# Kernel optimization log

Hardware: AMD Instinct MI355X
Metric: run time of the kernel (lower is better)

Reference implementation:

```python
import jax, jax.numpy as jnp
import numpy as np

EPS = float(np.finfo(np.float32).eps)  # torch.finfo(float32).eps


def _inv2x2(M):
    """Elementwise inverse of 2x2 complex matrices. M: (..., 2, 2) complex."""
    det = M[..., 0, 0] * M[..., 1, 1] - M[..., 0, 1] * M[..., 1, 0]
    # matches torch _inv: conj(z) / |z|^2
    inv_det = jnp.conj(det) / (jnp.abs(det) ** 2)
    row0 = jnp.stack([inv_det * M[..., 1, 1], -inv_det * M[..., 0, 1]], axis=-1)
    row1 = jnp.stack([-inv_det * M[..., 1, 0], inv_det * M[..., 0, 0]], axis=-1)
    return jnp.stack([row0, row1], axis=-2)


def _em(y, x, iterations):
    # y: (F, B, C, 2, S) real/imag; x: (F, B, C, 2)
    yc = y[..., 0, :] + 1j * y[..., 1, :]          # (F, B, C, S) complex
    xc = x[..., 0] + 1j * x[..., 1]                # (F, B, C)   complex
    nb_channels = yc.shape[2]
    reg = jnp.sqrt(jnp.asarray(EPS, jnp.float32)) * jnp.eye(
        nb_channels, dtype=yc.dtype)               # sqrt(eps)*I regularizer
    v = jnp.mean(jnp.abs(yc) ** 2, axis=2)         # (F, B, S)
    R = jnp.einsum('fbcs,fbds->bcds', yc, jnp.conj(yc))
    for _ in range(iterations):
        # E-step: PSD = channel-average power spectrogram
        v = jnp.mean(jnp.abs(yc) ** 2, axis=2)     # (F, B, S)
        # spatial covariance: sum_f y y^H / (eps + sum_f v)  -> (B, C, C, S)
        R = jnp.einsum('fbcs,fbds->bcds', yc, jnp.conj(yc))
        R = R / (EPS + jnp.sum(v, axis=0))[:, None, None, :]
        # mixture covariance Cxx = sqrt(eps)*I + sum_j v_j R_j  -> (F, B, C, C)
        Cxx = reg[None, None] + jnp.einsum('fbs,bcds->fbcd', v, R)
        inv_Cxx = _inv2x2(Cxx)
        # Wiener gain G_j = v_j * R_j @ inv_Cxx  -> (F, B, C, C, S)
        gain = jnp.einsum('fbs,bcks,fbkd->fbcds', v, R, inv_Cxx)
        # apply filter: y_j = G_j @ x
        yc = jnp.einsum('fbcds,fbd->fbcs', gain, xc)
    y_out = jnp.stack([jnp.real(yc), jnp.imag(yc)], axis=-2)   # (F, B, C, 2, S)
    R_out = jnp.stack([jnp.real(R), jnp.imag(R)], axis=-2)     # (B, C, C, 2, S)
    return y_out, v, R_out


def setup_inputs() -> dict:
    key = jax.random.key(0)
    k1, k2 = jax.random.split(key)
    F, B, C, S = 1000, 2049, 2, 4
    y = jax.random.normal(k1, (F, B, C, 2, S), dtype=jnp.float32)
    x = jax.random.normal(k2, (F, B, C, 2), dtype=jnp.float32)
    return {"y": y, "x": x, "iterations": 2}


def reference(y, x, iterations):
    return _em(y, x, iterations)
```

## Files before the change

### kernel.cpp

```cpp
#include <hip/hip_runtime.h>

#define FDIM 1000
#define BDIM 2049
#define NTH  256
#define FS   8
#define FT   125
#define BT   16
#define NBT  129
#define GRID (NBT * FS)

#define V_OFF 32784000ull
#define R_OFF 40980000ull

#define P2_OFF ((size_t)BDIM * FS * 20)

#define EPSF 1.1920928955078125e-07f
#define REGC 3.4526698300124393e-04f

__global__ __launch_bounds__(NTH) void k1_power(
    const float* __restrict__ y, float* __restrict__ v, float* __restrict__ part1)
{
    const int btile = blockIdx.x / FS;
    const int fs    = blockIdx.x % FS;
    const int tid   = threadIdx.x;
    const int bs    = tid & 15;
    const int fi    = tid >> 4;
    const int wid   = tid >> 6;
    const int b     = btile * BT + bs;
    const bool vb   = (b < BDIM);

    float acc[20];
    #pragma unroll
    for (int j = 0; j < 20; ++j) acc[j] = 0.f;

    const int f0 = fs * FT;
    #pragma unroll
    for (int ii = 0; ii < 8; ++ii) {
        const int fo = ii * 16 + fi;
        if (fo < FT && vb) {
            const int f = f0 + fo;
            const size_t e = (size_t)f * BDIM + b;
            const float4* yp = reinterpret_cast<const float4*>(y) + e * 4;
            float4 a0 = yp[0], a1 = yp[1], a2 = yp[2], a3 = yp[3];
            float y0r[4] = {a0.x,a0.y,a0.z,a0.w};
            float y0i[4] = {a1.x,a1.y,a1.z,a1.w};
            float y1r[4] = {a2.x,a2.y,a2.z,a2.w};
            float y1i[4] = {a3.x,a3.y,a3.z,a3.w};
            float vv[4];
            #pragma unroll
            for (int s = 0; s < 4; ++s) {
                const float p0 = y0r[s]*y0r[s] + y0i[s]*y0i[s];
                const float p1 = y1r[s]*y1r[s] + y1i[s]*y1i[s];
                vv[s] = 0.5f * (p0 + p1);
                acc[s]    += p0;
                acc[4+s]  += p1;
                acc[8+s]  += y0r[s]*y1r[s] + y0i[s]*y1i[s];
                acc[12+s] += y0i[s]*y1r[s] - y0r[s]*y1i[s];
                acc[16+s] += vv[s];
            }
            reinterpret_cast<float4*>(v)[e] = make_float4(vv[0], vv[1], vv[2], vv[3]);
        }
    }
    #pragma unroll
    for (int j = 0; j < 20; ++j) {
        float t = acc[j];
        t += __shfl_xor(t, 16);
        t += __shfl_xor(t, 32);
        acc[j] = t;
    }
    __shared__ float red[4][16][20];
    if ((tid & 63) < 16) {
        #pragma unroll
        for (int j = 0; j < 20; ++j) red[wid][bs][j] = acc[j];
    }
    __syncthreads();
    for (int idx = tid; idx < 320; idx += NTH) {
        const int bss = idx & 15, j = idx >> 4;
        const int bb = btile * BT + bss;
        if (bb < BDIM)
            part1[((size_t)bb * FS + fs) * 20 + j] =
                red[0][bss][j] + red[1][bss][j] + red[2][bss][j] + red[3][bss][j];
    }
}

__global__ __launch_bounds__(NTH) void k3_em(
    const float* __restrict__ x, float* __restrict__ v,
    const float* __restrict__ part1, float* __restrict__ part2,
    const int* __restrict__ itp)
{
    const int btile = blockIdx.x / FS;
    const int fs    = blockIdx.x % FS;
    const int tid   = threadIdx.x;
    const int bs    = tid & 15;
    const int fi    = tid >> 4;
    const int wid   = tid >> 6;
    const int b     = btile * BT + bs;
    const bool vb   = (b < BDIM);
    const int iters = itp[0];

    __shared__ float rsumS[16][20];
    __shared__ float rnormS[16][16];
    for (int idx = tid; idx < 320; idx += NTH) {
        const int bss = idx & 15, j = idx >> 4;
        const int bb = btile * BT + bss;
        float s = 0.f;
        if (bb < BDIM) {
            #pragma unroll
            for (int q = 0; q < FS; ++q) s += part1[((size_t)bb * FS + q) * 20 + j];
        }
        rsumS[bss][j] = s;
    }
    __syncthreads();
    {
        const int bss = tid & 15, j = tid >> 4;
        rnormS[bss][j] = rsumS[bss][j] / (EPSF + rsumS[bss][16 + (j & 3)]);
    }
    __syncthreads();

    if (iters <= 1) {
        for (int idx = tid; idx < 320; idx += NTH) {
            const int bss = idx & 15, j = idx >> 4;
            const int bb = btile * BT + bss;
            if (bb < BDIM)
                part2[((size_t)bb * FS + fs) * 20 + j] = (fs == 0) ? rsumS[bss][j] : 0.f;
        }
        return;
    }

    float rn00[4], rn11[4], rn01r[4], rn01i[4];
    #pragma unroll
    for (int s = 0; s < 4; ++s) {
        rn00[s]=rnormS[bs][s]; rn11[s]=rnormS[bs][4+s];
        rn01r[s]=rnormS[bs][8+s]; rn01i[s]=rnormS[bs][12+s];
    }

    float acc[20];
    #pragma unroll
    for (int j = 0; j < 20; ++j) acc[j] = 0.f;

    const int f0 = fs * FT;
    #pragma unroll
    for (int ii = 0; ii < 8; ++ii) {
        const int fo = ii * 16 + fi;
        if (fo < FT && vb) {
            const int f = f0 + fo;
            const size_t e = (size_t)f * BDIM + b;
            float4 vv4 = reinterpret_cast<const float4*>(v)[e];
            float4 xv  = reinterpret_cast<const float4*>(x)[e];
            float v1[4] = {vv4.x, vv4.y, vv4.z, vv4.w};
            float c00 = REGC, c11 = REGC, c01r = 0.f, c01i = 0.f;
            #pragma unroll
            for (int s = 0; s < 4; ++s) {
                c00  += v1[s]*rn00[s];
                c11  += v1[s]*rn11[s];
                c01r += v1[s]*rn01r[s];
                c01i += v1[s]*rn01i[s];
            }
            const float det  = c00*c11 - (c01r*c01r + c01i*c01i);
            const float invd = det / (det*det);
            const float i00 = invd*c11, i11 = invd*c00;
            const float i01r = -invd*c01r, i01i = -invd*c01i;
            const float xr0 = xv.x, xi0 = xv.y, xr1 = xv.z, xi1 = xv.w;
            const float w0r = i00*xr0 + (i01r*xr1 - i01i*xi1);
            const float w0i = i00*xi0 + (i01r*xi1 + i01i*xr1);
            const float w1r = (i01r*xr0 + i01i*xi0) + i11*xr1;
            const float w1i = (i01r*xi0 - i01i*xr0) + i11*xi1;
            float v2[4];
            #pragma unroll
            for (int s = 0; s < 4; ++s) {
                const float vs = v1[s];
                const float y0r = vs*(rn00[s]*w0r + (rn01r[s]*w1r - rn01i[s]*w1i));
                const float y0i = vs*(rn00[s]*w0i + (rn01r[s]*w1i + rn01i[s]*w1r));
                const float y1r = vs*((rn01r[s]*w0r + rn01i[s]*w0i) + rn11[s]*w1r);
                const float y1i = vs*((rn01r[s]*w0i - rn01i[s]*w0r) + rn11[s]*w1i);
                const float p0 = y0r*y0r + y0i*y0i;
                const float p1 = y1r*y1r + y1i*y1i;
                v2[s] = 0.5f*(p0 + p1);
                acc[s]    += p0;
                acc[4+s]  += p1;
                acc[8+s]  += y0r*y1r + y0i*y1i;
                acc[12+s] += y0i*y1r - y0r*y1i;
                acc[16+s] += v2[s];
            }
            reinterpret_cast<float4*>(v)[e] = make_float4(v2[0], v2[1], v2[2], v2[3]);
        }
    }
    #pragma unroll
    for (int j = 0; j < 20; ++j) {
        float t = acc[j];
        t += __shfl_xor(t, 16);
        t += __shfl_xor(t, 32);
        acc[j] = t;
    }
    __shared__ float red[4][16][20];
    if ((tid & 63) < 16) {
        #pragma unroll
        for (int j = 0; j < 20; ++j) red[wid][bs][j] = acc[j];
    }
    __syncthreads();
    for (int idx = tid; idx < 320; idx += NTH) {
        const int bss = idx & 15, j = idx >> 4;
        const int bb = btile * BT + bss;
        if (bb < BDIM)
            part2[((size_t)bb * FS + fs) * 20 + j] =
                red[0][bss][j] + red[1][bss][j] + red[2][bss][j] + red[3][bss][j];
    }
}

__global__ __launch_bounds__(NTH) void k5_final(
    const float* __restrict__ y, const float* __restrict__ x, const float* __restrict__ v,
    const float* __restrict__ part2, float* __restrict__ yout, float* __restrict__ Rout,
    const int* __restrict__ itp)
{
    const int btile = blockIdx.x / FS;
    const int fs    = blockIdx.x % FS;
    const int tid   = threadIdx.x;
    const int bs    = tid & 15;
    const int fi    = tid >> 4;
    const int b     = btile * BT + bs;
    const bool vb   = (b < BDIM);
    const int iters = itp[0];

    __shared__ float rsumS[16][20];
    __shared__ float rnormS[16][16];
    for (int idx = tid; idx < 320; idx += NTH) {
        const int bss = idx & 15, j = idx >> 4;
        const int bb = btile * BT + bss;
        float s = 0.f;
        if (bb < BDIM) {
            #pragma unroll
            for (int q = 0; q < FS; ++q) s += part2[((size_t)bb * FS + q) * 20 + j];
        }
        rsumS[bss][j] = s;
    }
    __syncthreads();
    {
        const int bss = tid & 15, j = tid >> 4;
        rnormS[bss][j] = rsumS[bss][j] / (EPSF + rsumS[bss][16 + (j & 3)]);
    }
    __syncthreads();

    if (fs == 0) {
        for (int idx = tid; idx < 512; idx += NTH) {
            const int bss = idx >> 5, r = idx & 31;
            const int bb = btile * BT + bss;
            if (bb < BDIM) {
                const int c = (r>>4)&1, d = (r>>3)&1, ri = (r>>2)&1, s = r&3;
                const bool raw = (iters == 0);
                float val;
                if (c == d) {
                    val = ri ? 0.f : (raw ? rsumS[bss][(c?4:0)+s] : rnormS[bss][(c?4:0)+s]);
                } else {
                    const float re = raw ? rsumS[bss][8+s]  : rnormS[bss][8+s];
                    const float im = raw ? rsumS[bss][12+s] : rnormS[bss][12+s];
                    val = ri ? (c == 0 ? im : -im) : re;
                }
                Rout[(size_t)bb * 32 + r] = val;
            }
        }
    }

    const int f0 = fs * FT;
    if (iters == 0) {
        #pragma unroll
        for (int ii = 0; ii < 8; ++ii) {
            const int fo = ii * 16 + fi;
            if (fo < FT && vb) {
                const size_t e = (size_t)(f0 + fo) * BDIM + b;
                const float4* yp = reinterpret_cast<const float4*>(y) + e * 4;
                float4* op = reinterpret_cast<float4*>(yout) + e * 4;
                op[0] = yp[0]; op[1] = yp[1]; op[2] = yp[2]; op[3] = yp[3];
            }
        }
        return;
    }

    float rn00[4], rn11[4], rn01r[4], rn01i[4];
    #pragma unroll
    for (int s = 0; s < 4; ++s) {
        rn00[s]=rnormS[bs][s]; rn11[s]=rnormS[bs][4+s];
        rn01r[s]=rnormS[bs][8+s]; rn01i[s]=rnormS[bs][12+s];
    }

    #pragma unroll
    for (int ii = 0; ii < 8; ++ii) {
        const int fo = ii * 16 + fi;
        if (fo < FT && vb) {
            const int f = f0 + fo;
            const size_t e = (size_t)f * BDIM + b;
            float4 vv4 = reinterpret_cast<const float4*>(v)[e];
            float4 xv  = reinterpret_cast<const float4*>(x)[e];
            float vcur[4] = {vv4.x, vv4.y, vv4.z, vv4.w};
            float c00 = REGC, c11 = REGC, c01r = 0.f, c01i = 0.f;
            #pragma unroll
            for (int s = 0; s < 4; ++s) {
                c00  += vcur[s]*rn00[s];
                c11  += vcur[s]*rn11[s];
                c01r += vcur[s]*rn01r[s];
                c01i += vcur[s]*rn01i[s];
            }
            const float det  = c00*c11 - (c01r*c01r + c01i*c01i);
            const float invd = det / (det*det);
            const float i00 = invd*c11, i11 = invd*c00;
            const float i01r = -invd*c01r, i01i = -invd*c01i;
            const float xr0 = xv.x, xi0 = xv.y, xr1 = xv.z, xi1 = xv.w;
            const float w0r = i00*xr0 + (i01r*xr1 - i01i*xi1);
            const float w0i = i00*xi0 + (i01r*xi1 + i01i*xr1);
            const float w1r = (i01r*xr0 + i01i*xi0) + i11*xr1;
            const float w1i = (i01r*xi0 - i01i*xr0) + i11*xi1;
            float o0r[4], o0i[4], o1r[4], o1i[4];
            #pragma unroll
            for (int s = 0; s < 4; ++s) {
                const float vs = vcur[s];
                o0r[s] = vs*(rn00[s]*w0r + (rn01r[s]*w1r - rn01i[s]*w1i));
                o0i[s] = vs*(rn00[s]*w0i + (rn01r[s]*w1i + rn01i[s]*w1r));
                o1r[s] = vs*((rn01r[s]*w0r + rn01i[s]*w0i) + rn11[s]*w1r);
                o1i[s] = vs*((rn01r[s]*w0i - rn01i[s]*w0r) + rn11[s]*w1i);
            }
            float4* op = reinterpret_cast<float4*>(yout) + e * 4;
            op[0] = make_float4(o0r[0], o0r[1], o0r[2], o0r[3]);
            op[1] = make_float4(o0i[0], o0i[1], o0i[2], o0i[3]);
            op[2] = make_float4(o1r[0], o1r[1], o1r[2], o1r[3]);
            op[3] = make_float4(o1i[0], o1i[1], o1i[2], o1i[3]);
        }
    }
}

extern "C" void kernel_launch(void* const* d_in, const int* in_sizes, int n_in,
                              void* d_out, int out_size, void* d_ws, size_t ws_size,
                              hipStream_t stream) {
    const float* y   = (const float*)d_in[0];
    const float* x   = (const float*)d_in[1];
    const int*   itp = (const int*)d_in[2];
    float* out   = (float*)d_out;
    float* vreg  = out + V_OFF;
    float* Rreg  = out + R_OFF;
    float* part1 = (float*)d_ws;
    float* part2 = part1 + P2_OFF;

    k1_power<<<GRID, NTH, 0, stream>>>(y, vreg, part1);
    k3_em   <<<GRID, NTH, 0, stream>>>(x, vreg, part1, part2, itp);
    k5_final<<<GRID, NTH, 0, stream>>>(y, x, vreg, part2, out, Rreg, itp);
}
```

Baseline: 334.8 us.

## Fuse three EM passes into one cooperative kernel with register-resident power

Replaces the three-kernel pipeline with a single cooperative-groups kernel that uses grid-wide syncs between the covariance reduction stages. Each thread keeps its per-frequency power values in registers (21 rows × 4 sources) across the passes, so the intermediate v array is no longer written and re-read from global memory. The grid is resized to 3 frequency splits so every block can be co-resident, with a fallback to the original kernels when cooperative launch is unavailable. In exchange it adds grid-sync cost, lower parallelism per b-tile, high register pressure (launch_bounds 256,2) and per-call device attribute queries.

```diff
diff --git a/kernel.cpp b/kernel.cpp
--- a/kernel.cpp
+++ b/kernel.cpp
@@ -1,95 +1,40 @@
 #include <hip/hip_runtime.h>
+#include <hip/hip_cooperative_groups.h>
+
+namespace cg = cooperative_groups;
 
 #define FDIM 1000
 #define BDIM 2049
 #define NTH  256
-#define FS   8
-#define FT   125
 #define BT   16
 #define NBT  129
-#define GRID (NBT * FS)
+
+#define CFS   3
+#define CFT   336
+#define CNII  21
+#define CGRID (NBT * CFS)
+
+#define FFS   8
+#define FFT   125
+#define FGRID (NBT * FFS)
 
 #define V_OFF 32784000ull
 #define R_OFF 40980000ull
 
-#define P2_OFF ((size_t)BDIM * FS * 20)
+#define P2_OFF ((size_t)BDIM * 8 * 20)
 
 #define EPSF 1.1920928955078125e-07f
 #define REGC 3.4526698300124393e-04f
 
-__global__ __launch_bounds__(NTH) void k1_power(
-    const float* __restrict__ y, float* __restrict__ v, float* __restrict__ part1)
-{
-    const int btile = blockIdx.x / FS;
-    const int fs    = blockIdx.x % FS;
-    const int tid   = threadIdx.x;
-    const int bs    = tid & 15;
-    const int fi    = tid >> 4;
-    const int wid   = tid >> 6;
-    const int b     = btile * BT + bs;
-    const bool vb   = (b < BDIM);
-
-    float acc[20];
-    #pragma unroll
-    for (int j = 0; j < 20; ++j) acc[j] = 0.f;
-
-    const int f0 = fs * FT;
-    #pragma unroll
-    for (int ii = 0; ii < 8; ++ii) {
-        const int fo = ii * 16 + fi;
-        if (fo < FT && vb) {
-            const int f = f0 + fo;
-            const size_t e = (size_t)f * BDIM + b;
-            const float4* yp = reinterpret_cast<const float4*>(y) + e * 4;
-            float4 a0 = yp[0], a1 = yp[1], a2 = yp[2], a3 = yp[3];
-            float y0r[4] = {a0.x,a0.y,a0.z,a0.w};
-            float y0i[4] = {a1.x,a1.y,a1.z,a1.w};
-            float y1r[4] = {a2.x,a2.y,a2.z,a2.w};
-            float y1i[4] = {a3.x,a3.y,a3.z,a3.w};
-            float vv[4];
-            #pragma unroll
-            for (int s = 0; s < 4; ++s) {
-                const float p0 = y0r[s]*y0r[s] + y0i[s]*y0i[s];
-                const float p1 = y1r[s]*y1r[s] + y1i[s]*y1i[s];
-                vv[s] = 0.5f * (p0 + p1);
-                acc[s]    += p0;
-                acc[4+s]  += p1;
-                acc[8+s]  += y0r[s]*y1r[s] + y0i[s]*y1i[s];
-                acc[12+s] += y0i[s]*y1r[s] - y0r[s]*y1i[s];
-                acc[16+s] += vv[s];
-            }
-            reinterpret_cast<float4*>(v)[e] = make_float4(vv[0], vv[1], vv[2], vv[3]);
-        }
-    }
-    #pragma unroll
-    for (int j = 0; j < 20; ++j) {
-        float t = acc[j];
-        t += __shfl_xor(t, 16);
-        t += __shfl_xor(t, 32);
-        acc[j] = t;
-    }
-    __shared__ float red[4][16][20];
-    if ((tid & 63) < 16) {
-        #pragma unroll
-        for (int j = 0; j < 20; ++j) red[wid][bs][j] = acc[j];
-    }
-    __syncthreads();
-    for (int idx = tid; idx < 320; idx += NTH) {
-        const int bss = idx & 15, j = idx >> 4;
-        const int bb = btile * BT + bss;
-        if (bb < BDIM)
-            part1[((size_t)bb * FS + fs) * 20 + j] =
-                red[0][bss][j] + red[1][bss][j] + red[2][bss][j] + red[3][bss][j];
-    }
-}
-
-__global__ __launch_bounds__(NTH) void k3_em(
-    const float* __restrict__ x, float* __restrict__ v,
-    const float* __restrict__ part1, float* __restrict__ part2,
+__global__ __launch_bounds__(NTH, 2) void k_fused(
+    const float* __restrict__ y, const float* __restrict__ x,
+    float* __restrict__ yout, float* __restrict__ vout, float* __restrict__ Rout,
+    float* __restrict__ part1, float* __restrict__ part2,
     const int* __restrict__ itp)
 {
-    const int btile = blockIdx.x / FS;
-    const int fs    = blockIdx.x % FS;
+    cg::grid_group gg = cg::this_grid();
+    const int btile = blockIdx.x / CFS;
+    const int fs    = blockIdx.x % CFS;
     const int tid   = threadIdx.x;
     const int bs    = tid & 15;
     const int fi    = tid >> 4;
@@ -97,16 +42,72 @@
     const int b     = btile * BT + bs;
     const bool vb   = (b < BDIM);
     const int iters = itp[0];
-
+    const int f0    = fs * CFT;
+
+    __shared__ float red[4][16][20];
     __shared__ float rsumS[16][20];
     __shared__ float rnormS[16][16];
+
+    float vst[CNII][4];
+    float acc[20];
+    #pragma unroll
+    for (int j = 0; j < 20; ++j) acc[j] = 0.f;
+
+    #pragma unroll
+    for (int ii = 0; ii < CNII; ++ii) {
+        const int f = f0 + ii * 16 + fi;
+        #pragma unroll
+        for (int s = 0; s < 4; ++s) vst[ii][s] = 0.f;
+        if ((f < FDIM) && vb) {
+            const size_t e = (size_t)f * BDIM + b;
+            const float4* yp = reinterpret_cast<const float4*>(y) + e * 4;
+            const float4 a0 = yp[0], a1 = yp[1], a2 = yp[2], a3 = yp[3];
+            const float y0r[4] = {a0.x,a0.y,a0.z,a0.w};
+            const float y0i[4] = {a1.x,a1.y,a1.z,a1.w};
+            const float y1r[4] = {a2.x,a2.y,a2.z,a2.w};
+            const float y1i[4] = {a3.x,a3.y,a3.z,a3.w};
+            #pragma unroll
+            for (int s = 0; s < 4; ++s) {
+                const float p0 = y0r[s]*y0r[s] + y0i[s]*y0i[s];
+                const float p1 = y1r[s]*y1r[s] + y1i[s]*y1i[s];
+                vst[ii][s] = 0.5f * (p0 + p1);
+                acc[s]    += p0;
+                acc[4+s]  += p1;
+                acc[8+s]  += y0r[s]*y1r[s] + y0i[s]*y1i[s];
+                acc[12+s] += y0i[s]*y1r[s] - y0r[s]*y1i[s];
+                acc[16+s] += vst[ii][s];
+            }
+        }
+    }
+    #pragma unroll
+    for (int j = 0; j < 20; ++j) {
+        float t = acc[j];
+        t += __shfl_xor(t, 16);
+        t += __shfl_xor(t, 32);
+        acc[j] = t;
+    }
+    if ((tid & 63) < 16) {
+        #pragma unroll
+        for (int j = 0; j < 20; ++j) red[wid][bs][j] = acc[j];
+    }
+    __syncthreads();
+    for (int idx = tid; idx < 320; idx += NTH) {
+        const int bss = idx & 15, j = idx >> 4;
+        const int bb = btile * BT + bss;
+        if (bb < BDIM)
+            part1[((size_t)bb * CFS + fs) * 20 + j] =
+                red[0][bss][j] + red[1][bss][j] + red[2][bss][j] + red[3][bss][j];
+    }
+
+    gg.sync();
+
     for (int idx = tid; idx < 320; idx += NTH) {
         const int bss = idx & 15, j = idx >> 4;
         const int bb = btile * BT + bss;
         float s = 0.f;
         if (bb < BDIM) {
             #pragma unroll
-            for (int q = 0; q < FS; ++q) s += part1[((size_t)bb * FS + q) * 20 + j];
+            for (int q = 0; q < CFS; ++q) s += part1[((size_t)bb * CFS + q) * 20 + j];
         }
         rsumS[bss][j] = s;
     }
@@ -117,119 +118,95 @@
     }
     __syncthreads();
 
-    if (iters <= 1) {
+    if (iters >= 2) {
+        float rn00[4], rn11[4], rn01r[4], rn01i[4];
+        #pragma unroll
+        for (int s = 0; s < 4; ++s) {
+            rn00[s]=rnormS[bs][s]; rn11[s]=rnormS[bs][4+s];
+            rn01r[s]=rnormS[bs][8+s]; rn01i[s]=rnormS[bs][12+s];
+        }
+        #pragma unroll
+        for (int j = 0; j < 20; ++j) acc[j] = 0.f;
+
+        #pragma unroll
+        for (int ii = 0; ii < CNII; ++ii) {
+            const int f = f0 + ii * 16 + fi;
+            if ((f < FDIM) && vb) {
+                const size_t e = (size_t)f * BDIM + b;
+                const float4 xv = reinterpret_cast<const float4*>(x)[e];
+                float c00 = REGC, c11 = REGC, c01r = 0.f, c01i = 0.f;
+                #pragma unroll
+                for (int s = 0; s < 4; ++s) {
+                    c00  += vst[ii][s]*rn00[s];
+                    c11  += vst[ii][s]*rn11[s];
+                    c01r += vst[ii][s]*rn01r[s];
+                    c01i += vst[ii][s]*rn01i[s];
+                }
+                const float det  = c00*c11 - (c01r*c01r + c01i*c01i);
+                const float invd = det / (det*det);
+                const float i00 = invd*c11, i11 = invd*c00;
+                const float i01r = -invd*c01r, i01i = -invd*c01i;
+                const float xr0 = xv.x, xi0 = xv.y, xr1 = xv.z, xi1 = xv.w;
+                const float w0r = i00*xr0 + (i01r*xr1 - i01i*xi1);
+                const float w0i = i00*xi0 + (i01r*xi1 + i01i*xr1);
+                const float w1r = (i01r*xr0 + i01i*xi0) + i11*xr1;
+                const float w1i = (i01r*xi0 - i01i*xr0) + i11*xi1;
+                #pragma unroll
+                for (int s = 0; s < 4; ++s) {
+                    const float vs = vst[ii][s];
+                    const float y0r = vs*(rn00[s]*w0r + (rn01r[s]*w1r - rn01i[s]*w1i));
+                    const float y0i = vs*(rn00[s]*w0i + (rn01r[s]*w1i + rn01i[s]*w1r));
+                    const float y1r = vs*((rn01r[s]*w0r + rn01i[s]*w0i) + rn11[s]*w1r);
+                    const float y1i = vs*((rn01r[s]*w0i - rn01i[s]*w0r) + rn11[s]*w1i);
+                    const float p0 = y0r*y0r + y0i*y0i;
+                    const float p1 = y1r*y1r + y1i*y1i;
+                    const float v2 = 0.5f*(p0 + p1);
+                    vst[ii][s] = v2;
+                    acc[s]    += p0;
+                    acc[4+s]  += p1;
+                    acc[8+s]  += y0r*y1r + y0i*y1i;
+                    acc[12+s] += y0i*y1r - y0r*y1i;
+                    acc[16+s] += v2;
+                }
+            }
+        }
+        #pragma unroll
+        for (int j = 0; j < 20; ++j) {
+            float t = acc[j];
+            t += __shfl_xor(t, 16);
+            t += __shfl_xor(t, 32);
+            acc[j] = t;
+        }
+        if ((tid & 63) < 16) {
+            #pragma unroll
+            for (int j = 0; j < 20; ++j) red[wid][bs][j] = acc[j];
+        }
+        __syncthreads();
         for (int idx = tid; idx < 320; idx += NTH) {
             const int bss = idx & 15, j = idx >> 4;
             const int bb = btile * BT + bss;
             if (bb < BDIM)
-                part2[((size_t)bb * FS + fs) * 20 + j] = (fs == 0) ? rsumS[bss][j] : 0.f;
-        }
-        return;
-    }
-
-    float rn00[4], rn11[4], rn01r[4], rn01i[4];
-    #pragma unroll
-    for (int s = 0; s < 4; ++s) {
-        rn00[s]=rnormS[bs][s]; rn11[s]=rnormS[bs][4+s];
-        rn01r[s]=rnormS[bs][8+s]; rn01i[s]=rnormS[bs][12+s];
-    }
-
-    float acc[20];
-    #pragma unroll
-    for (int j = 0; j < 20; ++j) acc[j] = 0.f;
-
-    const int f0 = fs * FT;
-    #pragma unroll
-    for (int ii = 0; ii < 8; ++ii) {
-        const int fo = ii * 16 + fi;
-        if (fo < FT && vb) {
-            const int f = f0 + fo;
-            const size_t e = (size_t)f * BDIM + b;
-            float4 vv4 = reinterpret_cast<const float4*>(v)[e];
-            float4 xv  = reinterpret_cast<const float4*>(x)[e];
-            float v1[4] = {vv4.x, vv4.y, vv4.z, vv4.w};
-            float c00 = REGC, c11 = REGC, c01r = 0.f, c01i = 0.f;
-            #pragma unroll
-            for (int s = 0; s < 4; ++s) {
-                c00  += v1[s]*rn00[s];
-                c11  += v1[s]*rn11[s];
-                c01r += v1[s]*rn01r[s];
-                c01i += v1[s]*rn01i[s];
-            }
-            const float det  = c00*c11 - (c01r*c01r + c01i*c01i);
-            const float invd = det / (det*det);
-            const float i00 = invd*c11, i11 = invd*c00;
-            const float i01r = -invd*c01r, i01i = -invd*c01i;
-            const float xr0 = xv.x, xi0 = xv.y, xr1 = xv.z, xi1 = xv.w;
-            const float w0r = i00*xr0 + (i01r*xr1 - i01i*xi1);
-            const float w0i = i00*xi0 + (i01r*xi1 + i01i*xr1);
-            const float w1r = (i01r*xr0 + i01i*xi0) + i11*xr1;
-            const float w1i = (i01r*xi0 - i01i*xr0) + i11*xi1;
-            float v2[4];
-            #pragma unroll
-            for (int s = 0; s < 4; ++s) {
-                const float vs = v1[s];
-                const float y0r = vs*(rn00[s]*w0r + (rn01r[s]*w1r - rn01i[s]*w1i));
-                const float y0i = vs*(rn00[s]*w0i + (rn01r[s]*w1i + rn01i[s]*w1r));
-                const float y1r = vs*((rn01r[s]*w0r + rn01i[s]*w0i) + rn11[s]*w1r);
-                const float y1i = vs*((rn01r[s]*w0i - rn01i[s]*w0r) + rn11[s]*w1i);
-                const float p0 = y0r*y0r + y0i*y0i;
-                const float p1 = y1r*y1r + y1i*y1i;
-                v2[s] = 0.5f*(p0 + p1);
-                acc[s]    += p0;
-                acc[4+s]  += p1;
-                acc[8+s]  += y0r*y1r + y0i*y1i;
-                acc[12+s] += y0i*y1r - y0r*y1i;
-                acc[16+s] += v2[s];
-            }
-            reinterpret_cast<float4*>(v)[e] = make_float4(v2[0], v2[1], v2[2], v2[3]);
-        }
-    }
-    #pragma unroll
-    for (int j = 0; j < 20; ++j) {
-        float t = acc[j];
-        t += __shfl_xor(t, 16);
-        t += __shfl_xor(t, 32);
-        acc[j] = t;
-    }
-    __shared__ float red[4][16][20];
-    if ((tid & 63) < 16) {
-        #pragma unroll
-        for (int j = 0; j < 20; ++j) red[wid][bs][j] = acc[j];
-    }
-    __syncthreads();
-    for (int idx = tid; idx < 320; idx += NTH) {
-        const int bss = idx & 15, j = idx >> 4;
-        const int bb = btile * BT + bss;
-        if (bb < BDIM)
-            part2[((size_t)bb * FS + fs) * 20 + j] =
-                red[0][bss][j] + red[1][bss][j] + red[2][bss][j] + red[3][bss][j];
-    }
-}
-
-__global__ __launch_bounds__(NTH) void k5_final(
-    const float* __restrict__ y, const float* __restrict__ x, const float* __restrict__ v,
-    const float* __restrict__ part2, float* __restrict__ yout, float* __restrict__ Rout,
-    const int* __restrict__ itp)
-{
-    const int btile = blockIdx.x / FS;
-    const int fs    = blockIdx.x % FS;
-    const int tid   = threadIdx.x;
-    const int bs    = tid & 15;
-    const int fi    = tid >> 4;
-    const int b     = btile * BT + bs;
-    const bool vb   = (b < BDIM);
-    const int iters = itp[0];
-
-    __shared__ float rsumS[16][20];
-    __shared__ float rnormS[16][16];
+                part2[((size_t)bb * CFS + fs) * 20 + j] =
+                    red[0][bss][j] + red[1][bss][j] + red[2][bss][j] + red[3][bss][j];
+        }
+    } else {
+        for (int idx = tid; idx < 320; idx += NTH) {
+            const int bss = idx & 15, j = idx >> 4;
+            const int bb = btile * BT + bss;
+            if (bb < BDIM)
+                part2[((size_t)bb * CFS + fs) * 20 + j] = (fs == 0) ? rsumS[bss][j] : 0.f;
+        }
+    }
+
+    gg.sync();
+
     for (int idx = tid; idx < 320; idx += NTH) {
         const int bss = idx & 15, j = idx >> 4;
         const int bb = btile * BT + bss;
         float s = 0.f;
         if (bb < BDIM) {
             #pragma unroll
-            for (int q = 0; q < FS; ++q) s += part2[((size_t)bb * FS + q) * 20 + j];
+            for (int q = 0; q < CFS; ++q) s += part2[((size_t)bb * CFS + q) * 20 + j];
         }
         rsumS[bss][j] = s;
     }
@@ -260,12 +237,321 @@
         }
     }
 
-    const int f0 = fs * FT;
+    if (iters == 0) {
+        #pragma unroll
+        for (int ii = 0; ii < CNII; ++ii) {
+            const int f = f0 + ii * 16 + fi;
+            if ((f < FDIM) && vb) {
+                const size_t e = (size_t)f * BDIM + b;
+                const float4* yp = reinterpret_cast<const float4*>(y) + e * 4;
+                float4* op = reinterpret_cast<float4*>(yout) + e * 4;
+                op[0] = yp[0]; op[1] = yp[1]; op[2] = yp[2]; op[3] = yp[3];
+                reinterpret_cast<float4*>(vout)[e] =
+                    make_float4(vst[ii][0], vst[ii][1], vst[ii][2], vst[ii][3]);
+            }
+        }
+        return;
+    }
+
+    float rn00[4], rn11[4], rn01r[4], rn01i[4];
+    #pragma unroll
+    for (int s = 0; s < 4; ++s) {
+        rn00[s]=rnormS[bs][s]; rn11[s]=rnormS[bs][4+s];
+        rn01r[s]=rnormS[bs][8+s]; rn01i[s]=rnormS[bs][12+s];
+    }
+
+    #pragma unroll
+    for (int ii = 0; ii < CNII; ++ii) {
+        const int f = f0 + ii * 16 + fi;
+        if ((f < FDIM) && vb) {
+            const size_t e = (size_t)f * BDIM + b;
+            const float4 xv = reinterpret_cast<const float4*>(x)[e];
+            float c00 = REGC, c11 = REGC, c01r = 0.f, c01i = 0.f;
+            #pragma unroll
+            for (int s = 0; s < 4; ++s) {
+                c00  += vst[ii][s]*rn00[s];
+                c11  += vst[ii][s]*rn11[s];
+                c01r += vst[ii][s]*rn01r[s];
+                c01i += vst[ii][s]*rn01i[s];
+            }
+            const float det  = c00*c11 - (c01r*c01r + c01i*c01i);
+            const float invd = det / (det*det);
+            const float i00 = invd*c11, i11 = invd*c00;
+            const float i01r = -invd*c01r, i01i = -invd*c01i;
+            const float xr0 = xv.x, xi0 = xv.y, xr1 = xv.z, xi1 = xv.w;
+            const float w0r = i00*xr0 + (i01r*xr1 - i01i*xi1);
+            const float w0i = i00*xi0 + (i01r*xi1 + i01i*xr1);
+            const float w1r = (i01r*xr0 + i01i*xi0) + i11*xr1;
+            const float w1i = (i01r*xi0 - i01i*xr0) + i11*xi1;
+            float o0r[4], o0i[4], o1r[4], o1i[4];
+            #pragma unroll
+            for (int s = 0; s < 4; ++s) {
+                const float vs = vst[ii][s];
+                o0r[s] = vs*(rn00[s]*w0r + (rn01r[s]*w1r - rn01i[s]*w1i));
+                o0i[s] = vs*(rn00[s]*w0i + (rn01r[s]*w1i + rn01i[s]*w1r));
+                o1r[s] = vs*((rn01r[s]*w0r + rn01i[s]*w0i) + rn11[s]*w1r);
+                o1i[s] = vs*((rn01r[s]*w0i - rn01i[s]*w0r) + rn11[s]*w1i);
+            }
+            float4* op = reinterpret_cast<float4*>(yout) + e * 4;
+            op[0] = make_float4(o0r[0], o0r[1], o0r[2], o0r[3]);
+            op[1] = make_float4(o0i[0], o0i[1], o0i[2], o0i[3]);
+            op[2] = make_float4(o1r[0], o1r[1], o1r[2], o1r[3]);
+            op[3] = make_float4(o1i[0], o1i[1], o1i[2], o1i[3]);
+            reinterpret_cast<float4*>(vout)[e] =
+                make_float4(vst[ii][0], vst[ii][1], vst[ii][2], vst[ii][3]);
+        }
+    }
+}
+
+__global__ __launch_bounds__(NTH) void k1_power(
+    const float* __restrict__ y, float* __restrict__ v, float* __restrict__ part1)
+{
+    const int btile = blockIdx.x / FFS;
+    const int fs    = blockIdx.x % FFS;
+    const int tid   = threadIdx.x;
+    const int bs    = tid & 15;
+    const int fi    = tid >> 4;
+    const int wid   = tid >> 6;
+    const int b     = btile * BT + bs;
+    const bool vb   = (b < BDIM);
+
+    float acc[20];
+    #pragma unroll
+    for (int j = 0; j < 20; ++j) acc[j] = 0.f;
+
+    const int f0 = fs * FFT;
+    #pragma unroll
+    for (int ii = 0; ii < 8; ++ii) {
+        const int fo = ii * 16 + fi;
+        if (fo < FFT && vb) {
+            const int f = f0 + fo;
+            const size_t e = (size_t)f * BDIM + b;
+            const float4* yp = reinterpret_cast<const float4*>(y) + e * 4;
+            float4 a0 = yp[0], a1 = yp[1], a2 = yp[2], a3 = yp[3];
+            float y0r[4] = {a0.x,a0.y,a0.z,a0.w};
+            float y0i[4] = {a1.x,a1.y,a1.z,a1.w};
+            float y1r[4] = {a2.x,a2.y,a2.z,a2.w};
+            float y1i[4] = {a3.x,a3.y,a3.z,a3.w};
+            float vv[4];
+            #pragma unroll
+            for (int s = 0; s < 4; ++s) {
+                const float p0 = y0r[s]*y0r[s] + y0i[s]*y0i[s];
+                const float p1 = y1r[s]*y1r[s] + y1i[s]*y1i[s];
+                vv[s] = 0.5f * (p0 + p1);
+                acc[s]    += p0;
+                acc[4+s]  += p1;
+                acc[8+s]  += y0r[s]*y1r[s] + y0i[s]*y1i[s];
+                acc[12+s] += y0i[s]*y1r[s] - y0r[s]*y1i[s];
+                acc[16+s] += vv[s];
+            }
+            reinterpret_cast<float4*>(v)[e] = make_float4(vv[0], vv[1], vv[2], vv[3]);
+        }
+    }
+    #pragma unroll
+    for (int j = 0; j < 20; ++j) {
+        float t = acc[j];
+        t += __shfl_xor(t, 16);
+        t += __shfl_xor(t, 32);
+        acc[j] = t;
+    }
+    __shared__ float red[4][16][20];
+    if ((tid & 63) < 16) {
+        #pragma unroll
+        for (int j = 0; j < 20; ++j) red[wid][bs][j] = acc[j];
+    }
+    __syncthreads();
+    for (int idx = tid; idx < 320; idx += NTH) {
+        const int bss = idx & 15, j = idx >> 4;
+        const int bb = btile * BT + bss;
+        if (bb < BDIM)
+            part1[((size_t)bb * FFS + fs) * 20 + j] =
+                red[0][bss][j] + red[1][bss][j] + red[2][bss][j] + red[3][bss][j];
+    }
+}
+
+__global__ __launch_bounds__(NTH) void k3_em(
+    const float* __restrict__ x, float* __restrict__ v,
+    const float* __restrict__ part1, float* __restrict__ part2,
+    const int* __restrict__ itp)
+{
+    const int btile = blockIdx.x / FFS;
+    const int fs    = blockIdx.x % FFS;
+    const int tid   = threadIdx.x;
+    const int bs    = tid & 15;
+    const int fi    = tid >> 4;
+    const int wid   = tid >> 6;
+    const int b     = btile * BT + bs;
+    const bool vb   = (b < BDIM);
+    const int iters = itp[0];
+
+    __shared__ float rsumS[16][20];
+    __shared__ float rnormS[16][16];
+    for (int idx = tid; idx < 320; idx += NTH) {
+        const int bss = idx & 15, j = idx >> 4;
+        const int bb = btile * BT + bss;
+        float s = 0.f;
+        if (bb < BDIM) {
+            #pragma unroll
+            for (int q = 0; q < FFS; ++q) s += part1[((size_t)bb * FFS + q) * 20 + j];
+        }
+        rsumS[bss][j] = s;
+    }
+    __syncthreads();
+    {
+        const int bss = tid & 15, j = tid >> 4;
+        rnormS[bss][j] = rsumS[bss][j] / (EPSF + rsumS[bss][16 + (j & 3)]);
+    }
+    __syncthreads();
+
+    if (iters <= 1) {
+        for (int idx = tid; idx < 320; idx += NTH) {
+            const int bss = idx & 15, j = idx >> 4;
+            const int bb = btile * BT + bss;
+            if (bb < BDIM)
+                part2[((size_t)bb * FFS + fs) * 20 + j] = (fs == 0) ? rsumS[bss][j] : 0.f;
+        }
+        return;
+    }
+
+    float rn00[4], rn11[4], rn01r[4], rn01i[4];
+    #pragma unroll
+    for (int s = 0; s < 4; ++s) {
+        rn00[s]=rnormS[bs][s]; rn11[s]=rnormS[bs][4+s];
+        rn01r[s]=rnormS[bs][8+s]; rn01i[s]=rnormS[bs][12+s];
+    }
+
+    float acc[20];
+    #pragma unroll
+    for (int j = 0; j < 20; ++j) acc[j] = 0.f;
+
+    const int f0 = fs * FFT;
+    #pragma unroll
+    for (int ii = 0; ii < 8; ++ii) {
+        const int fo = ii * 16 + fi;
+        if (fo < FFT && vb) {
+            const int f = f0 + fo;
+            const size_t e = (size_t)f * BDIM + b;
+            float4 vv4 = reinterpret_cast<const float4*>(v)[e];
+            float4 xv  = reinterpret_cast<const float4*>(x)[e];
+            float v1[4] = {vv4.x, vv4.y, vv4.z, vv4.w};
+            float c00 = REGC, c11 = REGC, c01r = 0.f, c01i = 0.f;
+            #pragma unroll
+            for (int s = 0; s < 4; ++s) {
+                c00  += v1[s]*rn00[s];
+                c11  += v1[s]*rn11[s];
+                c01r += v1[s]*rn01r[s];
+                c01i += v1[s]*rn01i[s];
+            }
+            const float det  = c00*c11 - (c01r*c01r + c01i*c01i);
+            const float invd = det / (det*det);
+            const float i00 = invd*c11, i11 = invd*c00;
+            const float i01r = -invd*c01r, i01i = -invd*c01i;
+            const float xr0 = xv.x, xi0 = xv.y, xr1 = xv.z, xi1 = xv.w;
+            const float w0r = i00*xr0 + (i01r*xr1 - i01i*xi1);
+            const float w0i = i00*xi0 + (i01r*xi1 + i01i*xr1);
+            const float w1r = (i01r*xr0 + i01i*xi0) + i11*xr1;
+            const float w1i = (i01r*xi0 - i01i*xr0) + i11*xi1;
+            float v2[4];
+            #pragma unroll
+            for (int s = 0; s < 4; ++s) {
+                const float vs = v1[s];
+                const float y0r = vs*(rn00[s]*w0r + (rn01r[s]*w1r - rn01i[s]*w1i));
+                const float y0i = vs*(rn00[s]*w0i + (rn01r[s]*w1i + rn01i[s]*w1r));
+                const float y1r = vs*((rn01r[s]*w0r + rn01i[s]*w0i) + rn11[s]*w1r);
+                const float y1i = vs*((rn01r[s]*w0i - rn01i[s]*w0r) + rn11[s]*w1i);
+                const float p0 = y0r*y0r + y0i*y0i;
+                const float p1 = y1r*y1r + y1i*y1i;
+                v2[s] = 0.5f*(p0 + p1);
+                acc[s]    += p0;
+                acc[4+s]  += p1;
+                acc[8+s]  += y0r*y1r + y0i*y1i;
+                acc[12+s] += y0i*y1r - y0r*y1i;
+                acc[16+s] += v2[s];
+            }
+            reinterpret_cast<float4*>(v)[e] = make_float4(v2[0], v2[1], v2[2], v2[3]);
+        }
+    }
+    #pragma unroll
+    for (int j = 0; j < 20; ++j) {
+        float t = acc[j];
+        t += __shfl_xor(t, 16);
+        t += __shfl_xor(t, 32);
+        acc[j] = t;
+    }
+    __shared__ float red[4][16][20];
+    if ((tid & 63) < 16) {
+        #pragma unroll
+        for (int j = 0; j < 20; ++j) red[wid][bs][j] = acc[j];
+    }
+    __syncthreads();
+    for (int idx = tid; idx < 320; idx += NTH) {
+        const int bss = idx & 15, j = idx >> 4;
+        const int bb = btile * BT + bss;
+        if (bb < BDIM)
+            part2[((size_t)bb * FFS + fs) * 20 + j] =
+                red[0][bss][j] + red[1][bss][j] + red[2][bss][j] + red[3][bss][j];
+    }
+}
+
+__global__ __launch_bounds__(NTH) void k5_final(
+    const float* __restrict__ y, const float* __restrict__ x, const float* __restrict__ v,
+    const float* __restrict__ part2, float* __restrict__ yout, float* __restrict__ Rout,
+    const int* __restrict__ itp)
+{
+    const int btile = blockIdx.x / FFS;
+    const int fs    = blockIdx.x % FFS;
+    const int tid   = threadIdx.x;
+    const int bs    = tid & 15;
+    const int fi    = tid >> 4;
+    const int b     = btile * BT + bs;
+    const bool vb   = (b < BDIM);
+    const int iters = itp[0];
+
+    __shared__ float rsumS[16][20];
+    __shared__ float rnormS[16][16];
+    for (int idx = tid; idx < 320; idx += NTH) {
+        const int bss = idx & 15, j = idx >> 4;
+        const int bb = btile * BT + bss;
+        float s = 0.f;
+        if (bb < BDIM) {
+            #pragma unroll
+            for (int q = 0; q < FFS; ++q) s += part2[((size_t)bb * FFS + q) * 20 + j];
+        }
+        rsumS[bss][j] = s;
+    }
+    __syncthreads();
+    {
+        const int bss = tid & 15, j = tid >> 4;
+        rnormS[bss][j] = rsumS[bss][j] / (EPSF + rsumS[bss][16 + (j & 3)]);
+    }
+    __syncthreads();
+
+    if (fs == 0) {
+        for (int idx = tid; idx < 512; idx += NTH) {
+            const int bss = idx >> 5, r = idx & 31;
+            const int bb = btile * BT + bss;
+            if (bb < BDIM) {
+                const int c = (r>>4)&1, d = (r>>3)&1, ri = (r>>2)&1, s = r&3;
+                const bool raw = (iters == 0);
+                float val;
+                if (c == d) {
+                    val = ri ? 0.f : (raw ? rsumS[bss][(c?4:0)+s] : rnormS[bss][(c?4:0)+s]);
+                } else {
+                    const float re = raw ? rsumS[bss][8+s]  : rnormS[bss][8+s];
+                    const float im = raw ? rsumS[bss][12+s] : rnormS[bss][12+s];
+                    val = ri ? (c == 0 ? im : -im) : re;
+                }
+                Rout[(size_t)bb * 32 + r] = val;
+            }
+        }
+    }
+
+    const int f0 = fs * FFT;
     if (iters == 0) {
         #pragma unroll
         for (int ii = 0; ii < 8; ++ii) {
             const int fo = ii * 16 + fi;
-            if (fo < FT && vb) {
+            if (fo < FFT && vb) {
                 const size_t e = (size_t)(f0 + fo) * BDIM + b;
                 const float4* yp = reinterpret_cast<const float4*>(y) + e * 4;
                 float4* op = reinterpret_cast<float4*>(yout) + e * 4;
@@ -285,7 +571,7 @@
     #pragma unroll
     for (int ii = 0; ii < 8; ++ii) {
         const int fo = ii * 16 + fi;
-        if (fo < FT && vb) {
+        if (fo < FFT && vb) {
             const int f = f0 + fo;
             const size_t e = (size_t)f * BDIM + b;
             float4 vv4 = reinterpret_cast<const float4*>(v)[e];
@@ -338,7 +624,26 @@
     float* part1 = (float*)d_ws;
     float* part2 = part1 + P2_OFF;
 
-    k1_power<<<GRID, NTH, 0, stream>>>(y, vreg, part1);
-    k3_em   <<<GRID, NTH, 0, stream>>>(x, vreg, part1, part2, itp);
-    k5_final<<<GRID, NTH, 0, stream>>>(y, x, vreg, part2, out, Rreg, itp);
+    bool use_coop = false;
+    int dev = 0, coop = 0, ncu = 0, maxb = 0;
+    if (hipGetDevice(&dev) == hipSuccess &&
+        hipDeviceGetAttribute(&coop, hipDeviceAttributeCooperativeLaunch, dev) == hipSuccess &&
+        coop != 0 &&
+        hipDeviceGetAttribute(&ncu, hipDeviceAttributeMultiprocessorCount, dev) == hipSuccess &&
+        hipOccupancyMaxActiveBlocksPerMultiprocessor(&maxb, (const void*)k_fused, NTH, 0) == hipSuccess &&
+        (long long)maxb * (long long)ncu >= (long long)CGRID)
+        use_coop = true;
+
+    if (use_coop) {
+        void* args[] = {(void*)&y, (void*)&x, (void*)&out, (void*)&vreg, (void*)&Rreg,
+                        (void*)&part1, (void*)&part2, (void*)&itp};
+        if (hipLaunchCooperativeKernel((void*)k_fused, dim3(CGRID), dim3(NTH),
+                                       args, 0, stream) != hipSuccess)
+            use_coop = false;
+    }
+    if (!use_coop) {
+        k1_power<<<FGRID, NTH, 0, stream>>>(y, vreg, part1);
+        k3_em   <<<FGRID, NTH, 0, stream>>>(x, vreg, part1, part2, itp);
+        k5_final<<<FGRID, NTH, 0, stream>>>(y, x, vreg, part2, out, Rreg, itp);
+    }
 }
```

After: 336.6 us. Within noise of the previous version (+0.5%).
